# Performance work log

Hardware: AMD Instinct MI355X
Metric: run time of the kernel (lower is better)

Reference implementation:

```python
import jax, jax.numpy as jnp
import numpy as np

DECAY = 0.99
EPSILON = 1e-05
BETA = 0.25  # vq_commitment_beta


def setup_inputs() -> dict:
    key = jax.random.key(0)
    k1, k2, k3, k4 = jax.random.split(key, 4)
    N, dim, K = 32768, 512, 8192
    init_range = 1.0 / np.sqrt(dim)
    emb_w = jax.random.uniform(k3, (K, 2 * dim), dtype=jnp.float32,
                               minval=-init_range, maxval=init_range)
    return {
        "z_real": jax.random.normal(k1, (N, dim), dtype=jnp.float32),
        "z_imag": jax.random.normal(k2, (N, dim), dtype=jnp.float32),
        "emb_w": emb_w,
        "ema_cluster_size": jnp.zeros((K,), dtype=jnp.float32),
        "ema_w": emb_w.copy(),
    }


def reference(z_real, z_imag, emb_w, ema_cluster_size, ema_w):
    N, dim = z_real.shape
    K = emb_w.shape[0]
    z_flat = jnp.concatenate([z_real, z_imag], axis=-1)  # [N, 2*dim]

    # squared euclidean distances [N, K]
    x_sq = jnp.sum(z_flat * z_flat, axis=1, keepdims=True)
    y_sq = jnp.sum(emb_w * emb_w, axis=1)
    d = jnp.maximum(x_sq + y_sq - 2.0 * (z_flat @ emb_w.T), 0.0)
    indices = jnp.argmin(d, axis=-1)  # [N]
    z_q = emb_w[indices]              # [N, 2*dim]

    # EMA codebook update (training-mode buffer math, no grads)
    n_total = jnp.zeros((K,), z_flat.dtype).at[indices].add(1.0)
    new_cluster_size = ema_cluster_size * DECAY + (1.0 - DECAY) * n_total
    cs = new_cluster_size + EPSILON
    cs = cs + (cs < 1.0).astype(cs.dtype)
    dw = jnp.zeros((K, 2 * dim), z_flat.dtype).at[indices].add(z_flat)  # encodings.T @ z_flat
    new_ema_w = ema_w * DECAY + (1.0 - DECAY) * dw
    new_w = jnp.clip(new_ema_w / cs[:, None], -5.0, 5.0)

    loss_sample = BETA * jnp.mean((z_q - z_flat) ** 2, axis=-1)  # [N]

    # straight-through (forward value == z_q)
    z_q_st = z_flat + jax.lax.stop_gradient(z_q - z_flat)

    probs = n_total / N
    norm_entropy = -jnp.sum(probs * jnp.log(probs + 1e-10)) / np.log(float(K))

    z_q_r = z_q_st[..., :dim]
    z_q_i = z_q_st[..., dim:]
    return (z_q_r, z_q_i, loss_sample, indices, norm_entropy,
            new_w, new_cluster_size, new_ema_w)
```

## Files before the change

kernel.cpp:

```cpp
#include <hip/hip_runtime.h>
#include <hip/hip_bf16.h>

#define NROWS 32768
#define DIM   512
#define D2    1024
#define KCODE 8192
#define DECAYF 0.99f
#define OMD    0.01f
#define CANDCAP 16
#define ZMAX 6.0f
#define IRANGE 0.04419417382415922f
#define MARGIN_P (9200 << 7)

typedef __attribute__((ext_vector_type(4))) int   v4i;
typedef __attribute__((ext_vector_type(16))) int  i32x16;

#define WS_EMB8T   0u
#define WS_YSQ     8388608u
#define WS_NINT    8421376u
#define WS_ENT     8454144u
#define WS_FIDX    10682384u
#define WS_OFF     10813456u
#define WS_CUR     10846224u
#define WS_ROWLIST 10878992u

#define OUT_ZQR  0
#define OUT_ZQI  16777216
#define OUT_LOSS 33554432
#define OUT_IDX  33587200
#define OUT_ENT  33619968
#define OUT_NEWW 33619969
#define OUT_NCS  42008577
#define OUT_NEMA 42016769
#define PAIRS_OFF (OUT_NEWW + 1)

__device__ __forceinline__ float wredf(float v) {
    #pragma unroll
    for (int o = 32; o > 0; o >>= 1) v += __shfl_down(v, o, 64);
    return v;
}

__device__ __forceinline__ double wredd(double v) {
    #pragma unroll
    for (int o = 32; o > 0; o >>= 1) v += __shfl_down(v, o, 64);
    return __shfl(v, 0, 64);
}

__device__ __forceinline__ double ulp32_of(double v) {
    return scalbn(1.0, ilogb(v) - 23);
}

__device__ __forceinline__ void gload_lds16(const void* g, void* l) {
    __builtin_amdgcn_global_load_lds(
        (const __attribute__((address_space(1))) unsigned int*)(g),
        (__attribute__((address_space(3))) unsigned int*)(l), 16, 0, 0);
}

__device__ __forceinline__ int q4(float4 v, float s) {
    int a = (int)rintf(fminf(fmaxf(v.x * s, -127.f), 127.f));
    int b = (int)rintf(fminf(fmaxf(v.y * s, -127.f), 127.f));
    int c = (int)rintf(fminf(fmaxf(v.z * s, -127.f), 127.f));
    int d = (int)rintf(fminf(fmaxf(v.w * s, -127.f), 127.f));
    return (a & 255) | ((b & 255) << 8) | ((c & 255) << 16) | ((d & 255) << 24);
}

__global__ __launch_bounds__(256) void prep_emb(const float* __restrict__ emb,
                                                char* __restrict__ emb8t,
                                                int* __restrict__ ysq) {
    int wave = threadIdx.x >> 6, lane = threadIdx.x & 63;
    int k = blockIdx.x * 4 + wave;
    const float4* src = (const float4*)(emb + (size_t)k * D2);
    const float es = 127.0f / IRANGE;
    const float sfac_inv = 1.0f / (2.0f * (ZMAX / 127.0f) * (IRANGE / 127.0f));
    float s = 0.f;
    float4 v0 = src[lane * 4 + 0];
    float4 v1 = src[lane * 4 + 1];
    float4 v2 = src[lane * 4 + 2];
    float4 v3 = src[lane * 4 + 3];
    s += v0.x*v0.x + v0.y*v0.y + v0.z*v0.z + v0.w*v0.w;
    s += v1.x*v1.x + v1.y*v1.y + v1.z*v1.z + v1.w*v1.w;
    s += v2.x*v2.x + v2.y*v2.y + v2.z*v2.z + v2.w*v2.w;
    s += v3.x*v3.x + v3.y*v3.y + v3.z*v3.z + v3.w*v3.w;
    v4i pk; pk[0] = q4(v0, es); pk[1] = q4(v1, es); pk[2] = q4(v2, es); pk[3] = q4(v3, es);
    v4i* dst = (v4i*)(emb8t + (size_t)(k >> 5) * 32768 + (size_t)lane * 512 + (k & 31) * 16);
    *dst = pk;
    s = wredf(s);
    if (lane == 0) ysq[k] = (int)rintf(s * sfac_inv);
}

__global__ __launch_bounds__(512, 2) void argmin_gemm(
    const float* __restrict__ zr, const float* __restrict__ zi,
    const char* __restrict__ emb8t, const int* __restrict__ ysq,
    long long* __restrict__ pairs)
{
    __shared__ char bufs[4][32768];
    const int tid  = threadIdx.x;
    const int wave = tid >> 6, lane = tid & 63;
    const int colc = lane & 31;
    const int hh   = lane >> 5;
    const int rowblk = blockIdx.x >> 1;
    const int slice  = blockIdx.x & 1;

    const int arow = rowblk * 256 + wave * 32 + colc;
    const float zs = 127.0f / ZMAX;
    const float* zrp = zr + (size_t)arow * 512 + hh * 16;
    const float* zip = zi + (size_t)arow * 512 + hh * 16;
    v4i afrag[32];
    #pragma unroll
    for (int ft = 0; ft < 16; ++ft) {
        const float4* p = (const float4*)(zrp + ft * 32);
        v4i a; a[0] = q4(p[0], zs); a[1] = q4(p[1], zs); a[2] = q4(p[2], zs); a[3] = q4(p[3], zs);
        afrag[ft] = a;
    }
    #pragma unroll
    for (int ft = 0; ft < 16; ++ft) {
        const float4* p = (const float4*)(zip + ft * 32);
        v4i a; a[0] = q4(p[0], zs); a[1] = q4(p[1], zs); a[2] = q4(p[2], zs); a[3] = q4(p[3], zs);
        afrag[16 + ft] = a;
    }

    int tv0[16], tv1[16];
    #pragma unroll
    for (int g = 0; g < 16; ++g) { tv0[g] = 0x7FFFFFFF; tv1[g] = 0x7FFFFFFF; }

    const char* gslice = emb8t + (size_t)slice * 128 * 32768;
    const int* yslice = ysq + slice * 4096;

#define STAGE(bidx_, t_) do {                                                    \
        const char* gb = gslice + (size_t)(t_) * 32768 + wave * 4096             \
                       + (size_t)lane * 16;                                      \
        char* lb = &bufs[bidx_][0] + wave * 4096;                                \
        gload_lds16(gb,        lb);                                              \
        gload_lds16(gb + 1024, lb + 1024);                                       \
        gload_lds16(gb + 2048, lb + 2048);                                       \
        gload_lds16(gb + 3072, lb + 3072);                                       \
    } while (0)

    const int boff = colc * 16 + hh * 512;

    STAGE(0, 0);
    STAGE(1, 1);
    STAGE(2, 2);

    for (int h = 0; h < 128; ++h) {
        asm volatile("s_waitcnt vmcnt(8) lgkmcnt(0)" ::: "memory");
        __builtin_amdgcn_s_barrier();
        __builtin_amdgcn_sched_barrier(0);
        STAGE((h + 3) & 3, (h + 3) & 127);
        int ysv = yslice[h * 32 + colc];

        const char* bb = &bufs[h & 3][0] + boff;
        i32x16 accP, accQ;
        #pragma unroll
        for (int g = 0; g < 16; ++g) { accP[g] = 0; accQ[g] = 0; }
        __builtin_amdgcn_s_setprio(1);
        #pragma unroll
        for (int m = 0; m < 16; ++m) {
            v4i bP = *(const v4i*)(bb + (2 * m) * 1024);
            v4i bQ = *(const v4i*)(bb + (2 * m + 1) * 1024);
            accP = __builtin_amdgcn_mfma_i32_32x32x32_i8(afrag[2 * m],     bP, accP, 0, 0, 0);
            accQ = __builtin_amdgcn_mfma_i32_32x32x32_i8(afrag[2 * m + 1], bQ, accQ, 0, 0, 0);
        }
        __builtin_amdgcn_s_setprio(0);

        #pragma unroll
        for (int g = 0; g < 16; ++g) {
            int pk = ((ysv - accP[g] - accQ[g]) << 7) | h;
            tv1[g] = min(tv1[g], max(pk, tv0[g]));
            tv0[g] = min(tv0[g], pk);
        }
    }
#undef STAGE

    #pragma unroll
    for (int g = 0; g < 16; ++g) {
        int rloc = (g & 3) + 8 * (g >> 2) + 4 * hh;
        int rowg = rowblk * 256 + wave * 32 + rloc;
        size_t base = (size_t)rowg * 128 + slice * 64 + colc * 2;
        int t0 = tv0[g], t1 = tv1[g];
        int code0 = slice * 4096 + (t0 & 127) * 32 + colc;
        int code1 = slice * 4096 + (t1 & 127) * 32 + colc;
        pairs[base + 0] = ((long long)(unsigned)code0 << 32) | (unsigned)t0;
        pairs[base + 1] = ((long long)(unsigned)code1 << 32) | (unsigned)t1;
    }
}

__global__ __launch_bounds__(256) void cleanup(
    const float* __restrict__ zr, const float* __restrict__ zi,
    const float* __restrict__ emb, const long long* __restrict__ pairs,
    int* __restrict__ fidx, int* __restrict__ nint, float* __restrict__ out)
{
    __shared__ int candlds[4][CANDCAP];
    int wave = threadIdx.x >> 6, lane = threadIdx.x & 63;
    int r = blockIdx.x * 4 + wave;

    const long long* pr = pairs + (size_t)r * 128;
    long long p0 = pr[lane];
    long long p1 = pr[64 + lane];
    int v0v = (int)(unsigned)p0;
    int i0  = (int)(p0 >> 32);
    int v1v = (int)(unsigned)p1;
    int i1  = (int)(p1 >> 32);
    int m = min(v0v, v1v);
    #pragma unroll
    for (int o = 32; o > 0; o >>= 1) m = min(m, __shfl_xor(m, o, 64));
    int lim = m + MARGIN_P;
    unsigned long long m0 = __ballot(v0v < lim);
    unsigned long long m1 = __ballot(v1v < lim);
    int t0 = __popcll(m0);
    int cnt = t0 + __popcll(m1);
    if (cnt > CANDCAP) cnt = CANDCAP;
    unsigned long long below = (lane == 63) ? 0xFFFFFFFFFFFFFFFFull >> 1
                                            : ((1ull << lane) - 1);
    if (v0v < lim) {
        int pos = __popcll(m0 & below);
        if (pos < CANDCAP) candlds[wave][pos] = i0;
    }
    if (v1v < lim) {
        int pos = t0 + __popcll(m1 & below);
        if (pos < CANDCAP) candlds[wave][pos] = i1;
    }
    int best = candlds[wave][0];

    float zreg[16];
    #pragma unroll
    for (int p = 0; p < 4; ++p) {
        int d4 = p * 64 + lane;
        const float4* zp = (d4 < 128) ? (const float4*)(zr + (size_t)r * 512)
                                      : ((const float4*)(zi + (size_t)r * 512) - 128);
        float4 zv = zp[d4];
        zreg[p * 4 + 0] = zv.x; zreg[p * 4 + 1] = zv.y;
        zreg[p * 4 + 2] = zv.z; zreg[p * 4 + 3] = zv.w;
    }

    if (cnt > 1) {
        double xs = 0.0;
        #pragma unroll
        for (int j = 0; j < 16; ++j) xs += (double)zreg[j] * (double)zreg[j];
        xs = wredd(xs);
        double uS = ulp32_of(xs);

        double bD = 1e300; int bi = 1 << 30;
        for (int i = 0; i < cnt; ++i) {
            int cdx = candlds[wave][i];
            const float4* ep = (const float4*)(emb + (size_t)cdx * 1024);
            double ys = 0.0, tt = 0.0;
            #pragma unroll
            for (int p = 0; p < 4; ++p) {
                float4 ev = ep[p * 64 + lane];
                float q0 = ev.x * ev.x, q1 = ev.y * ev.y, q2 = ev.z * ev.z, q3 = ev.w * ev.w;
                ys += (double)q0 + (double)q1 + (double)q2 + (double)q3;
                tt += (double)zreg[p * 4 + 0] * (double)ev.x
                    + (double)zreg[p * 4 + 1] * (double)ev.y
                    + (double)zreg[p * 4 + 2] * (double)ev.z
                    + (double)zreg[p * 4 + 3] * (double)ev.w;
            }
            ys = wredd(ys);
            tt = wredd(tt);
            float y32 = (float)ys;
            float t32 = (float)tt;
            double dex = xs + ys - 2.0 * tt;
            double ud = ulp32_of(dex);
            double D = rint((double)y32 / uS) * uS - rint(2.0 * (double)t32 / ud) * ud;
            if (D < bD || (D == bD && cdx < bi)) { bD = D; bi = cdx; }
        }
        best = bi;
    }

    const float4* ep = (const float4*)(emb + (size_t)best * 1024);
    float acc = 0.f;
    #pragma unroll
    for (int p = 0; p < 4; ++p) {
        int d4 = p * 64 + lane;
        float4 ev = ep[d4];
        float dx = ev.x - zreg[p * 4 + 0]; acc += dx * dx;
        float dy = ev.y - zreg[p * 4 + 1]; acc += dy * dy;
        float dz = ev.z - zreg[p * 4 + 2]; acc += dz * dz;
        float dw = ev.w - zreg[p * 4 + 3]; acc += dw * dw;
        float4* op = (d4 < 128) ? (float4*)(out + OUT_ZQR + (size_t)r * 512)
                                : ((float4*)(out + OUT_ZQI + (size_t)r * 512) - 128);
        op[d4] = ev;
    }
    acc = wredf(acc);
    if (lane == 0) {
        fidx[r] = best;
        out[OUT_IDX + r] = (float)best;
        out[OUT_LOSS + r] = 0.25f * acc * (1.f / 1024.f);
        atomicAdd(nint + best, 1);
    }
}

__global__ __launch_bounds__(256) void scan_codes(const int* __restrict__ nint,
                                                  int* __restrict__ off,
                                                  int* __restrict__ cur) {
    __shared__ int part[256];
    int tid = threadIdx.x;
    int base = tid * 32;
    int loc[32];
    int s = 0;
    #pragma unroll
    for (int j = 0; j < 32; ++j) { loc[j] = s; s += nint[base + j]; }
    part[tid] = s;
    __syncthreads();
    for (int o = 1; o < 256; o <<= 1) {
        int t = (tid >= o) ? part[tid - o] : 0;
        __syncthreads();
        part[tid] += t;
        __syncthreads();
    }
    int excl = part[tid] - s;
    #pragma unroll
    for (int j = 0; j < 32; ++j) {
        off[base + j] = excl + loc[j];
        cur[base + j] = 0;
    }
}

__global__ __launch_bounds__(256) void fill_rows(const int* __restrict__ fidx,
                                                 const int* __restrict__ off,
                                                 int* __restrict__ cur,
                                                 int* __restrict__ rowlist) {
    int r = blockIdx.x * 256 + threadIdx.x;
    int idx = fidx[r];
    int pos = atomicAdd(cur + idx, 1);
    rowlist[off[idx] + pos] = r;
}

__global__ __launch_bounds__(256) void ema_update(
    const float* __restrict__ zr, const float* __restrict__ zi,
    const float* __restrict__ emaw, const float* __restrict__ emacs,
    const int* __restrict__ nint, const int* __restrict__ off,
    const int* __restrict__ rowlist, float* __restrict__ out,
    float* __restrict__ entacc)
{
    int k = blockIdx.x;
    int tid = threadIdx.x;
    int cnt = nint[k];
    int o0 = off[k];
    float ax = 0.f, ay = 0.f, az = 0.f, aw = 0.f;
    for (int i = 0; i < cnt; ++i) {
        int r = rowlist[o0 + i];
        float4 zv = (tid < 128) ? ((const float4*)(zr + (size_t)r * 512))[tid]
                                : ((const float4*)(zi + (size_t)r * 512))[tid - 128];
        ax += zv.x; ay += zv.y; az += zv.z; aw += zv.w;
    }
    float4 ew = ((const float4*)(emaw + (size_t)k * 1024))[tid];
    float4 nem;
    nem.x = DECAYF * ew.x + OMD * ax;
    nem.y = DECAYF * ew.y + OMD * ay;
    nem.z = DECAYF * ew.z + OMD * az;
    nem.w = DECAYF * ew.w + OMD * aw;
    ((float4*)(out + OUT_NEMA + (size_t)k * 1024))[tid] = nem;
    float ncs = DECAYF * emacs[k] + OMD * (float)cnt;
    float cs = ncs + 1e-5f;
    if (cs < 1.f) cs += 1.f;
    float inv = 1.f / cs;
    float4 w;
    w.x = fminf(fmaxf(nem.x * inv, -5.f), 5.f);
    w.y = fminf(fmaxf(nem.y * inv, -5.f), 5.f);
    w.z = fminf(fmaxf(nem.z * inv, -5.f), 5.f);
    w.w = fminf(fmaxf(nem.w * inv, -5.f), 5.f);
    ((float4*)(out + OUT_NEWW + (size_t)k * 1024))[tid] = w;
    if (tid == 0) {
        out[OUT_NCS + k] = ncs;
        float p = (float)cnt / 32768.f;
        atomicAdd(entacc, -p * logf(p + 1e-10f));
    }
}

__global__ void ent_fin(const float* __restrict__ entacc, float* __restrict__ out) {
    if (threadIdx.x == 0) out[OUT_ENT] = entacc[0] / logf(8192.f);
}

extern "C" void kernel_launch(void* const* d_in, const int* in_sizes, int n_in,
                              void* d_out, int out_size, void* d_ws, size_t ws_size,
                              hipStream_t stream)
{
    const float* zr    = (const float*)d_in[0];
    const float* zi    = (const float*)d_in[1];
    const float* emb   = (const float*)d_in[2];
    const float* emacs = (const float*)d_in[3];
    const float* emaw  = (const float*)d_in[4];
    float* out = (float*)d_out;
    char* ws = (char*)d_ws;

    char*  emb8t   = (char*)(ws + WS_EMB8T);
    int*   ysq     = (int*)(ws + WS_YSQ);
    int*   nint    = (int*)(ws + WS_NINT);
    float* entacc  = (float*)(ws + WS_ENT);
    int*   fidx    = (int*)(ws + WS_FIDX);
    int*   off     = (int*)(ws + WS_OFF);
    int*   cur     = (int*)(ws + WS_CUR);
    int*   rowlist = (int*)(ws + WS_ROWLIST);
    long long* pairs = (long long*)(out + PAIRS_OFF);

    hipMemsetAsync(ws + WS_NINT, 0, 32768 + 16, stream);

    prep_emb   <<<2048, 256, 0, stream>>>(emb, emb8t, ysq);
    argmin_gemm<<<256,  512, 0, stream>>>(zr, zi, emb8t, ysq, pairs);
    cleanup    <<<8192, 256, 0, stream>>>(zr, zi, emb, pairs, fidx, nint, out);
    scan_codes <<<1,    256, 0, stream>>>(nint, off, cur);
    fill_rows  <<<128,  256, 0, stream>>>(fidx, off, cur, rowlist);
    ema_update <<<8192, 256, 0, stream>>>(zr, zi, emaw, emacs, nint, off, rowlist, out, entacc);
    ent_fin    <<<1,    64,  0, stream>>>(entacc, out);
}
```

Baseline: 527.6 us.

## Halve argmin GEMM block size and switch to double-buffered LDS pipeline

The argmin GEMM now runs 256-thread blocks that each cover 128 rows, doubling the grid to 512 blocks. The 4-deep LDS ring with explicit vmcnt waits becomes a 2-buffer scheme with __syncthreads after every codebook tile. This cuts LDS per block so more blocks can be resident, but it doubles how often each codebook tile is loaded per row and removes the deeper prefetch.

Measured after the change: 545.5 us. 1.03x slower.

```diff
diff --git a/kernel.cpp b/kernel.cpp
--- a/kernel.cpp
+++ b/kernel.cpp
@@ -88,12 +88,12 @@
     if (lane == 0) ysq[k] = (int)rintf(s * sfac_inv);
 }
 
-__global__ __launch_bounds__(512, 2) void argmin_gemm(
+__global__ __launch_bounds__(256, 2) void argmin_gemm(
     const float* __restrict__ zr, const float* __restrict__ zi,
     const char* __restrict__ emb8t, const int* __restrict__ ysq,
     long long* __restrict__ pairs)
 {
-    __shared__ char bufs[4][32768];
+    __shared__ char bufs[2][32768];
     const int tid  = threadIdx.x;
     const int wave = tid >> 6, lane = tid & 63;
     const int colc = lane & 31;
@@ -101,7 +101,7 @@
     const int rowblk = blockIdx.x >> 1;
     const int slice  = blockIdx.x & 1;
 
-    const int arow = rowblk * 256 + wave * 32 + colc;
+    const int arow = rowblk * 128 + wave * 32 + colc;
     const float zs = 127.0f / ZMAX;
     const float* zrp = zr + (size_t)arow * 512 + hh * 16;
     const float* zip = zi + (size_t)arow * 512 + hh * 16;
@@ -126,30 +126,26 @@
     const char* gslice = emb8t + (size_t)slice * 128 * 32768;
     const int* yslice = ysq + slice * 4096;
 
-#define STAGE(bidx_, t_) do {                                                    \
-        const char* gb = gslice + (size_t)(t_) * 32768 + wave * 4096             \
+#define STAGE(dstbuf, t_) do {                                                   \
+        const char* gb = gslice + (size_t)(t_) * 32768 + wave * 8192             \
                        + (size_t)lane * 16;                                      \
-        char* lb = &bufs[bidx_][0] + wave * 4096;                                \
-        gload_lds16(gb,        lb);                                              \
-        gload_lds16(gb + 1024, lb + 1024);                                       \
-        gload_lds16(gb + 2048, lb + 2048);                                       \
-        gload_lds16(gb + 3072, lb + 3072);                                       \
+        char* lb = (dstbuf) + wave * 8192;                                       \
+        _Pragma("unroll")                                                        \
+        for (int q = 0; q < 8; ++q)                                              \
+            gload_lds16(gb + q * 1024, lb + q * 1024);                           \
     } while (0)
 
     const int boff = colc * 16 + hh * 512;
 
-    STAGE(0, 0);
-    STAGE(1, 1);
-    STAGE(2, 2);
-
-    for (int h = 0; h < 128; ++h) {
-        asm volatile("s_waitcnt vmcnt(8) lgkmcnt(0)" ::: "memory");
-        __builtin_amdgcn_s_barrier();
-        __builtin_amdgcn_sched_barrier(0);
-        STAGE((h + 3) & 3, (h + 3) & 127);
-        int ysv = yslice[h * 32 + colc];
-
-        const char* bb = &bufs[h & 3][0] + boff;
+    STAGE(bufs[0], 0);
+    __syncthreads();
+
+    for (int c = 0; c < 128; ++c) {
+        const int cur = c & 1;
+        if (c + 1 < 128) STAGE(bufs[cur ^ 1], c + 1);
+        int ysv = yslice[c * 32 + colc];
+
+        const char* bb = &bufs[cur][0] + boff;
         i32x16 accP, accQ;
         #pragma unroll
         for (int g = 0; g < 16; ++g) { accP[g] = 0; accQ[g] = 0; }
@@ -165,17 +161,18 @@
 
         #pragma unroll
         for (int g = 0; g < 16; ++g) {
-            int pk = ((ysv - accP[g] - accQ[g]) << 7) | h;
+            int pk = ((ysv - accP[g] - accQ[g]) << 7) | c;
             tv1[g] = min(tv1[g], max(pk, tv0[g]));
             tv0[g] = min(tv0[g], pk);
         }
+        __syncthreads();
     }
 #undef STAGE
 
     #pragma unroll
     for (int g = 0; g < 16; ++g) {
         int rloc = (g & 3) + 8 * (g >> 2) + 4 * hh;
-        int rowg = rowblk * 256 + wave * 32 + rloc;
+        int rowg = rowblk * 128 + wave * 32 + rloc;
         size_t base = (size_t)rowg * 128 + slice * 64 + colc * 2;
         int t0 = tv0[g], t1 = tv1[g];
         int code0 = slice * 4096 + (t0 & 127) * 32 + colc;
@@ -397,7 +394,7 @@
     hipMemsetAsync(ws + WS_NINT, 0, 32768 + 16, stream);
 
     prep_emb   <<<2048, 256, 0, stream>>>(emb, emb8t, ysq);
-    argmin_gemm<<<256,  512, 0, stream>>>(zr, zi, emb8t, ysq, pairs);
+    argmin_gemm<<<512,  256, 0, stream>>>(zr, zi, emb8t, ysq, pairs);
     cleanup    <<<8192, 256, 0, stream>>>(zr, zi, emb, pairs, fidx, nint, out);
     scan_codes <<<1,    256, 0, stream>>>(nint, off, cur);
     fill_rows  <<<128,  256, 0, stream>>>(fidx, off, cur, rowlist);
```
